# Performance work log

Hardware: AMD Instinct MI355X
Metric: run time of the kernel (lower is better)

Reference implementation:

```python
import jax, jax.numpy as jnp
import numpy as np

BN_EPS = 1e-5


def setup_inputs() -> dict:
    key = jax.random.key(0)
    ks = jax.random.split(key, 8)
    N, E, D, G, L = 50000, 800000, 128, 64, 4
    x = jax.random.normal(ks[0], (N, D), dtype=jnp.float32)
    edge_index = jax.random.randint(ks[1], (2, E), 0, N, dtype=jnp.int64)
    batch = jnp.sort(jax.random.randint(ks[2], (N,), 0, G, dtype=jnp.int64))
    sc = 1.0 / np.sqrt(D)
    W1 = jax.random.normal(ks[3], (L, D, D), dtype=jnp.float32) * sc
    b1 = jnp.zeros((L, D), dtype=jnp.float32)
    gamma = jnp.ones((L, D), dtype=jnp.float32)
    beta = jnp.zeros((L, D), dtype=jnp.float32)
    W2 = jax.random.normal(ks[4], (L, D, D), dtype=jnp.float32) * sc
    b2 = jnp.zeros((L, D), dtype=jnp.float32)
    return {"x": x, "edge_index": edge_index, "batch": batch,
            "W1": W1, "b1": b1, "gamma": gamma, "beta": beta,
            "W2": W2, "b2": b2}


def _segment_mean(vals, ids, num_segments):
    s = jax.ops.segment_sum(vals, ids, num_segments=num_segments)
    cnt = jax.ops.segment_sum(jnp.ones((vals.shape[0],), vals.dtype), ids,
                              num_segments=num_segments)
    return s / jnp.clip(cnt, 1.0)[:, None]


def reference(x, edge_index, batch, W1, b1, gamma, beta, W2, b2):
    N = x.shape[0]
    L = W1.shape[0]
    G = 64  # number of graphs
    src, dst = edge_index[0], edge_index[1]  # source_to_target flow
    # in-degree counts for scatter-mean (fixed across layers)
    deg = jax.ops.segment_sum(jnp.ones((src.shape[0],), x.dtype), dst,
                              num_segments=N)
    deg = jnp.clip(deg, 1.0)[:, None]
    h = x
    node_pool = jnp.zeros((N, W1.shape[2]), x.dtype)
    g_pool = jnp.zeros((G, W1.shape[2]), x.dtype)
    for l in range(L):
        # scatter-mean neighbor aggregation, GIN update with eps=0
        agg = jax.ops.segment_sum(h[src], dst, num_segments=N) / deg
        z = h + agg
        # MLP: Linear -> BatchNorm1d (batch stats) -> ReLU -> Linear
        z = z @ W1[l] + b1[l]
        mu = jnp.mean(z, axis=0)
        var = jnp.mean(jnp.square(z - mu), axis=0)  # biased, as in torch BN
        z = gamma[l] * (z - mu) * jax.lax.rsqrt(var + BN_EPS) + beta[l]
        z = jax.nn.relu(z)
        h = z @ W2[l] + b2[l]
        node_pool = node_pool + h
        g_pool = g_pool + _segment_mean(h, batch, G)
    return node_pool, g_pool
```

## Files before the change

kernel.cpp:

```cpp
#include <hip/hip_runtime.h>

#define D 128
#define GNUM 64
#define LNUM 4
#define BN_EPS 1e-5f
#define EPB 16384
#define SH_MAX 12544

typedef short bf16x8 __attribute__((ext_vector_type(8)));
typedef float f32x4 __attribute__((ext_vector_type(4)));
typedef unsigned short u16x8 __attribute__((ext_vector_type(8)));
typedef unsigned short u16x4 __attribute__((ext_vector_type(4)));

__device__ __forceinline__ float bf2f(unsigned short u) {
  union { unsigned int i; float f; } v; v.i = ((unsigned int)u) << 16; return v.f;
}
__device__ __forceinline__ unsigned short f2bf(float f) {
  union { float f; unsigned int i; } v; v.f = f;
  unsigned int b = v.i;
  return (unsigned short)((b + 0x7FFFu + ((b >> 16) & 1u)) >> 16);
}

__global__ __launch_bounds__(256) void k_hist(const int* __restrict__ ei, int E,
                                              int B, int nbin, int* __restrict__ hist) {
  __shared__ int lh[256];
  int b = blockIdx.x, tx = threadIdx.x;
  lh[tx] = 0;
  __syncthreads();
  int s = b * EPB, e = min(s + EPB, E);
  for (int j = s + tx; j < e; j += 256) atomicAdd(&lh[ei[(size_t)E + j] >> 8], 1);
  __syncthreads();
  if (tx < nbin) hist[tx * B + b] = lh[tx];
}

__global__ __launch_bounds__(1024) void k_hscan(const int* __restrict__ hist, int M,
                                                int* __restrict__ off,
                                                int* __restrict__ rowptr, int N, int E) {
  __shared__ int sh[SH_MAX];
  __shared__ int sh2[1024];
  int tx = threadIdx.x;
  int chunk = (M + 1023) / 1024;
  for (int i = 0; i < chunk; ++i) {
    int idx = tx * chunk + i;
    sh[idx] = (idx < M) ? hist[idx] : 0;
  }
  __syncthreads();
  int s = 0;
  for (int i = 0; i < chunk; ++i) s += sh[tx * chunk + i];
  sh2[tx] = s;
  __syncthreads();
  for (int o = 1; o < 1024; o <<= 1) {
    int u = (tx >= o) ? sh2[tx - o] : 0;
    __syncthreads();
    sh2[tx] += u;
    __syncthreads();
  }
  int run = (tx == 0) ? 0 : sh2[tx - 1];
  for (int i = 0; i < chunk; ++i) {
    int idx = tx * chunk + i;
    if (idx < M) { int v = sh[idx]; off[idx] = run; run += v; }
  }
  if (tx == 0) rowptr[N] = E;
}

__global__ __launch_bounds__(256) void k_scatter(const int* __restrict__ ei, int E,
                                                 int B, int nbin,
                                                 const int* __restrict__ off,
                                                 int2* __restrict__ sorted) {
  __shared__ int cur[256];
  int b = blockIdx.x, tx = threadIdx.x;
  if (tx < nbin) cur[tx] = off[tx * B + b];
  __syncthreads();
  int s = b * EPB, e = min(s + EPB, E);
  for (int j = s + tx; j < e; j += 256) {
    int d = ei[(size_t)E + j];
    int sc = ei[j];
    int p = atomicAdd(&cur[d >> 8], 1);
    sorted[p] = make_int2(d, sc);
  }
}

__global__ __launch_bounds__(256) void k_build(const int2* __restrict__ sorted,
                                               const int* __restrict__ off,
                                               int B, int nbin, int E, int N,
                                               int* __restrict__ rowptr,
                                               int* __restrict__ col) {
  __shared__ int cnt[256], excl[256], cur[256];
  int beta = blockIdx.x, tx = threadIdx.x;
  int s = off[beta * B];
  int e = (beta + 1 < nbin) ? off[(beta + 1) * B] : E;
  cnt[tx] = 0;
  __syncthreads();
  for (int j = s + tx; j < e; j += 256) atomicAdd(&cnt[sorted[j].x & 255], 1);
  __syncthreads();
  int v = cnt[tx];
  excl[tx] = v;
  __syncthreads();
  for (int o = 1; o < 256; o <<= 1) {
    int u = (tx >= o) ? excl[tx - o] : 0;
    __syncthreads();
    excl[tx] += u;
    __syncthreads();
  }
  int ex = excl[tx] - v;
  int n = beta * 256 + tx;
  if (n < N) rowptr[n] = s + ex;
  cur[tx] = s + ex;
  __syncthreads();
  for (int j = s + tx; j < e; j += 256) {
    int2 p = sorted[j];
    int q = atomicAdd(&cur[p.x & 255], 1);
    col[q] = p.y;
  }
}

__global__ void k_bounds(const int* __restrict__ batch, int N, int* __restrict__ bound) {
  int g = threadIdx.x;
  if (g > GNUM) return;
  int lo = 0, hi = N;
  while (lo < hi) { int mid = (lo + hi) >> 1; if (batch[mid] < g) lo = mid + 1; else hi = mid; }
  bound[g] = lo;
}

__global__ void k_prep_x(const float* __restrict__ x, unsigned short* __restrict__ hx, int total4) {
  int i = blockIdx.x * 256 + threadIdx.x;
  if (i < total4) {
    f32x4 v = ((const f32x4*)x)[i];
    u16x4 o; o[0] = f2bf(v[0]); o[1] = f2bf(v[1]); o[2] = f2bf(v[2]); o[3] = f2bf(v[3]);
    ((u16x4*)hx)[i] = o;
  }
}

__global__ __launch_bounds__(256) void k_prep_w(const float* __restrict__ W1,
                                                const float* __restrict__ W2,
                                                unsigned short* __restrict__ wt) {
  int l = blockIdx.x;
  const float* W = (l < LNUM) ? (W1 + (size_t)l * D * D) : (W2 + (size_t)(l - LNUM) * D * D);
  unsigned short* o = wt + (size_t)l * D * D;
#pragma unroll
  for (int i = 0; i < 64; ++i) {
    int idx = threadIdx.x + 256 * i;
    int k = idx >> 7, n = idx & 127;
    o[n * D + k] = f2bf(W[idx]);
  }
}

__global__ __launch_bounds__(256) void k_layer1(const unsigned short* __restrict__ hin,
                                                const int* __restrict__ rowptr,
                                                const int* __restrict__ col,
                                                const unsigned short* __restrict__ wt,
                                                const float* __restrict__ bias,
                                                unsigned short* __restrict__ t,
                                                float* __restrict__ partials, int N) {
  __shared__ union { unsigned short zt[64 * D]; float red[2 * 8 * D]; } uA;
  __shared__ union { unsigned short wl[D * D]; float out[64 * D]; } uB;
  int tx = threadIdx.x;
  int r0 = blockIdx.x * 64;
  const u16x8* wg = (const u16x8*)wt;
#pragma unroll
  for (int i = 0; i < 8; ++i) {
    int cid = tx + 256 * i;
    int row = cid >> 4, c16 = cid & 15;
    u16x8 v = wg[cid];
    *(u16x8*)((char*)uB.wl + row * 256 + ((c16 * 16) ^ ((row & 7) << 4))) = v;
  }
  int grp = tx >> 4, c = tx & 15;
  const u16x8* h8 = (const u16x8*)hin;
#pragma unroll
  for (int i = 0; i < 4; ++i) {
    int row = grp * 4 + i;
    int n = r0 + row;
    u16x8 o;
    if (n < N) {
      int e0 = rowptr[n], e1 = rowptr[n + 1];
      f32x4 s0 = {0.f,0.f,0.f,0.f}, s1 = {0.f,0.f,0.f,0.f};
      f32x4 t0 = {0.f,0.f,0.f,0.f}, t1 = {0.f,0.f,0.f,0.f};
      int j = e0;
      for (; j + 3 < e1; j += 4) {
        u16x8 v0 = h8[(size_t)col[j] * 16 + c];
        u16x8 v1 = h8[(size_t)col[j + 1] * 16 + c];
        u16x8 v2 = h8[(size_t)col[j + 2] * 16 + c];
        u16x8 v3 = h8[(size_t)col[j + 3] * 16 + c];
#pragma unroll
        for (int k = 0; k < 4; ++k) {
          s0[k] += bf2f(v0[k]) + bf2f(v1[k]);
          s1[k] += bf2f(v0[4 + k]) + bf2f(v1[4 + k]);
          t0[k] += bf2f(v2[k]) + bf2f(v3[k]);
          t1[k] += bf2f(v2[4 + k]) + bf2f(v3[4 + k]);
        }
      }
      for (; j < e1; ++j) {
        u16x8 v0 = h8[(size_t)col[j] * 16 + c];
#pragma unroll
        for (int k = 0; k < 4; ++k) { s0[k] += bf2f(v0[k]); s1[k] += bf2f(v0[4 + k]); }
      }
      s0 += t0; s1 += t1;
      float inv = (e1 > e0) ? 1.f / (float)(e1 - e0) : 0.f;
      u16x8 hv = h8[(size_t)n * 16 + c];
#pragma unroll
      for (int k = 0; k < 4; ++k) {
        o[k] = f2bf(bf2f(hv[k]) + s0[k] * inv);
        o[4 + k] = f2bf(bf2f(hv[4 + k]) + s1[k] * inv);
      }
    } else {
      o = (u16x8){0, 0, 0, 0, 0, 0, 0, 0};
    }
    *(u16x8*)((char*)uA.zt + row * 256 + ((c * 16) ^ ((row & 7) << 4))) = o;
  }
  __syncthreads();
  int l = tx & 63, w = tx >> 6;
  int lm = l & 15, lg = l >> 4;
  f32x4 acc[8];
#pragma unroll
  for (int cc = 0; cc < 8; ++cc) { float bv = bias[cc * 16 + lm]; acc[cc] = (f32x4){bv, bv, bv, bv}; }
  int arow = 16 * w + lm;
  const char* zb = (const char*)uA.zt + arow * 256;
  int aswz = (arow & 7) << 4;
#pragma unroll
  for (int kt = 0; kt < 4; ++kt) {
    int koff = kt * 64 + lg * 16;
    bf16x8 af = *(const bf16x8*)(zb + (koff ^ aswz));
#pragma unroll
    for (int cc = 0; cc < 8; ++cc) {
      int n = cc * 16 + lm;
      bf16x8 bfr = *(const bf16x8*)((const char*)uB.wl + n * 256 + (koff ^ ((n & 7) << 4)));
      acc[cc] = __builtin_amdgcn_mfma_f32_16x16x32_bf16(af, bfr, acc[cc], 0, 0, 0);
    }
  }
  __syncthreads();
#pragma unroll
  for (int cc = 0; cc < 8; ++cc)
#pragma unroll
    for (int r = 0; r < 4; ++r)
      uB.out[(16 * w + 4 * lg + r) * D + cc * 16 + lm] = acc[cc][r];
  __syncthreads();
  int tc = tx & 31, tr = tx >> 5;
  f32x4 s = {0.f, 0.f, 0.f, 0.f}, q = {0.f, 0.f, 0.f, 0.f};
#pragma unroll
  for (int i = 0; i < 8; ++i) {
    int row = i * 8 + tr;
    f32x4 v = *(f32x4*)&uB.out[row * D + tc * 4];
    u16x4 o; o[0] = f2bf(v[0]); o[1] = f2bf(v[1]); o[2] = f2bf(v[2]); o[3] = f2bf(v[3]);
    *(u16x4*)(t + (size_t)(r0 + row) * D + tc * 4) = o;
    if (r0 + row < N) { s += v; q += v * v; }
  }
  *(f32x4*)&uA.red[tr * D + tc * 4] = s;
  *(f32x4*)&uA.red[8 * D + tr * D + tc * 4] = q;
  __syncthreads();
  int colx = tx & 127, which = tx >> 7;
  float S = 0.f;
#pragma unroll
  for (int j = 0; j < 8; ++j) S += uA.red[which * 8 * D + j * D + colx];
  partials[(size_t)blockIdx.x * 256 + tx] = S;
}

__global__ __launch_bounds__(256) void k_red1(const float* __restrict__ partials, int NB,
                                              float* __restrict__ partial2) {
  int tx = threadIdx.x;
  float S = 0.f;
  for (int b = blockIdx.x; b < NB; b += 64) S += partials[(size_t)b * 256 + tx];
  partial2[(size_t)blockIdx.x * 256 + tx] = S;
}

__global__ __launch_bounds__(256) void k_finalize(const float* __restrict__ partial2,
                                                  const float* __restrict__ gamma,
                                                  const float* __restrict__ beta,
                                                  float* __restrict__ stats, int N) {
  __shared__ float sh[256];
  int tx = threadIdx.x;
  float S = 0.f;
#pragma unroll 8
  for (int b = 0; b < 64; ++b) S += partial2[(size_t)b * 256 + tx];
  sh[tx] = S;
  __syncthreads();
  if (tx < D) {
    float mu = sh[tx] / (float)N;
    float var = sh[D + tx] / (float)N - mu * mu;
    float rstd = rsqrtf(fmaxf(var, 0.f) + BN_EPS);
    float A = gamma[tx] * rstd;
    stats[tx] = A;
    stats[D + tx] = beta[tx] - mu * A;
  }
}

__device__ __forceinline__ void gemm2_core(const unsigned short* t,
                                           const unsigned short* wt,
                                           const float* bias, const float* stats,
                                           unsigned short* at, unsigned short* wl,
                                           float* outbuf, int r0) {
  int tx = threadIdx.x;
  const u16x8* tg = (const u16x8*)(t + (size_t)r0 * D);
#pragma unroll
  for (int i = 0; i < 4; ++i) {
    int cid = tx + 256 * i;
    int row = cid >> 4, c16 = cid & 15;
    u16x8 v = tg[cid];
    int c0 = c16 * 8;
    f32x4 a0 = *(const f32x4*)&stats[c0];
    f32x4 a1 = *(const f32x4*)&stats[c0 + 4];
    f32x4 b0 = *(const f32x4*)&stats[D + c0];
    f32x4 b1v = *(const f32x4*)&stats[D + c0 + 4];
    u16x8 o;
    o[0] = f2bf(fmaxf(bf2f(v[0]) * a0[0] + b0[0], 0.f));
    o[1] = f2bf(fmaxf(bf2f(v[1]) * a0[1] + b0[1], 0.f));
    o[2] = f2bf(fmaxf(bf2f(v[2]) * a0[2] + b0[2], 0.f));
    o[3] = f2bf(fmaxf(bf2f(v[3]) * a0[3] + b0[3], 0.f));
    o[4] = f2bf(fmaxf(bf2f(v[4]) * a1[0] + b1v[0], 0.f));
    o[5] = f2bf(fmaxf(bf2f(v[5]) * a1[1] + b1v[1], 0.f));
    o[6] = f2bf(fmaxf(bf2f(v[6]) * a1[2] + b1v[2], 0.f));
    o[7] = f2bf(fmaxf(bf2f(v[7]) * a1[3] + b1v[3], 0.f));
    *(u16x8*)((char*)at + row * 256 + ((c16 * 16) ^ ((row & 7) << 4))) = o;
  }
  const u16x8* wg = (const u16x8*)wt;
#pragma unroll
  for (int i = 0; i < 8; ++i) {
    int cid = tx + 256 * i;
    int row = cid >> 4, c16 = cid & 15;
    u16x8 v = wg[cid];
    *(u16x8*)((char*)wl + row * 256 + ((c16 * 16) ^ ((row & 7) << 4))) = v;
  }
  __syncthreads();
  int l = tx & 63, w = tx >> 6;
  int lm = l & 15, lg = l >> 4;
  f32x4 acc[8];
#pragma unroll
  for (int c = 0; c < 8; ++c) { float bv = bias[c * 16 + lm]; acc[c] = (f32x4){bv, bv, bv, bv}; }
  int arow = 16 * w + lm;
  const char* ab = (const char*)at + arow * 256;
  int aswz = (arow & 7) << 4;
#pragma unroll
  for (int kt = 0; kt < 4; ++kt) {
    int koff = kt * 64 + lg * 16;
    bf16x8 af = *(const bf16x8*)(ab + (koff ^ aswz));
#pragma unroll
    for (int c = 0; c < 8; ++c) {
      int n = c * 16 + lm;
      bf16x8 bfr = *(const bf16x8*)((const char*)wl + n * 256 + (koff ^ ((n & 7) << 4)));
      acc[c] = __builtin_amdgcn_mfma_f32_16x16x32_bf16(af, bfr, acc[c], 0, 0, 0);
    }
  }
  __syncthreads();
#pragma unroll
  for (int c = 0; c < 8; ++c)
#pragma unroll
    for (int r = 0; r < 4; ++r)
      outbuf[(16 * w + 4 * lg + r) * D + c * 16 + lm] = acc[c][r];
  __syncthreads();
}

__global__ __launch_bounds__(256) void k_gemm2(const unsigned short* __restrict__ t,
                                               const unsigned short* __restrict__ wt,
                                               const float* __restrict__ bias,
                                               const float* __restrict__ stats,
                                               unsigned short* __restrict__ h, int N) {
  __shared__ unsigned short at[64 * D];
  __shared__ union { unsigned short wl[D * D]; float out[64 * D]; } uB;
  int tx = threadIdx.x;
  int r0 = blockIdx.x * 64;
  gemm2_core(t, wt, bias, stats, at, uB.wl, uB.out, r0);
  int tc = tx & 31, tr = tx >> 5;
#pragma unroll
  for (int i = 0; i < 8; ++i) {
    int row = i * 8 + tr;
    int gr = r0 + row;
    if (gr < N) {
      f32x4 v = *(f32x4*)&uB.out[row * D + tc * 4];
      u16x4 hb; hb[0] = f2bf(v[0]); hb[1] = f2bf(v[1]); hb[2] = f2bf(v[2]); hb[3] = f2bf(v[3]);
      *(u16x4*)(h + (size_t)gr * D + tc * 4) = hb;
    }
  }
}

__global__ __launch_bounds__(256) void k_gemm2_last(const unsigned short* __restrict__ t,
                                                    const unsigned short* __restrict__ wt,
                                                    const float* __restrict__ bias,
                                                    const float* __restrict__ stats,
                                                    const unsigned short* __restrict__ h0,
                                                    const unsigned short* __restrict__ h1,
                                                    const unsigned short* __restrict__ h2,
                                                    float* __restrict__ np, int N) {
  __shared__ unsigned short at[64 * D];
  __shared__ union { unsigned short wl[D * D]; float out[64 * D]; } uB;
  int tx = threadIdx.x;
  int r0 = blockIdx.x * 64;
  gemm2_core(t, wt, bias, stats, at, uB.wl, uB.out, r0);
  int tc = tx & 31, tr = tx >> 5;
#pragma unroll
  for (int i = 0; i < 8; ++i) {
    int row = i * 8 + tr;
    int gr = r0 + row;
    if (gr < N) {
      f32x4 v = *(f32x4*)&uB.out[row * D + tc * 4];
      size_t o4 = (size_t)gr * D + tc * 4;
      u16x4 a = *(const u16x4*)(h0 + o4);
      u16x4 b = *(const u16x4*)(h1 + o4);
      u16x4 cc = *(const u16x4*)(h2 + o4);
      f32x4 o;
#pragma unroll
      for (int k = 0; k < 4; ++k)
        o[k] = v[k] + (bf2f(a[k]) + bf2f(b[k])) + bf2f(cc[k]);
      *(f32x4*)(np + o4) = o;
    }
  }
}

__global__ __launch_bounds__(256) void k_gpool(const float* __restrict__ np,
                                               const int* __restrict__ bound,
                                               float* __restrict__ gp) {
  __shared__ float red[8 * D];
  int g = blockIdx.x;
  int s = bound[g], e = bound[g + 1];
  int tc = threadIdx.x & 31, tr = threadIdx.x >> 5;
  f32x4 a = {0.f, 0.f, 0.f, 0.f};
  for (int r = s + tr; r < e; r += 8)
    a += *(const f32x4*)(np + (size_t)r * D + tc * 4);
  *(f32x4*)&red[tr * D + tc * 4] = a;
  __syncthreads();
  if (threadIdx.x < D) {
    float v = 0.f;
#pragma unroll
    for (int j = 0; j < 8; ++j) v += red[j * D + threadIdx.x];
    float c = (float)(e - s);
    gp[(size_t)g * D + threadIdx.x] = v / fmaxf(c, 1.f);
  }
}

extern "C" void kernel_launch(void* const* d_in, const int* in_sizes, int n_in,
                              void* d_out, int out_size, void* d_ws,
                              size_t ws_size, hipStream_t stream) {
  const float* x = (const float*)d_in[0];
  const int* ei = (const int*)d_in[1];
  const int* batch = (const int*)d_in[2];
  const float* W1 = (const float*)d_in[3];
  const float* b1 = (const float*)d_in[4];
  const float* gamma = (const float*)d_in[5];
  const float* beta = (const float*)d_in[6];
  const float* W2 = (const float*)d_in[7];
  const float* b2 = (const float*)d_in[8];
  int N = in_sizes[0] / D;
  int E = in_sizes[1] / 2;
  int Npad = (N + 63) & ~63;
  int gb = Npad / 64;
  int B = (E + EPB - 1) / EPB;
  int nbin = (N + 255) / 256;
  int M = nbin * B;

  float* out = (float*)d_out;
  float* node_pool = out;
  float* g_pool = out + (size_t)N * D;

  char* wp = (char*)d_ws;
  unsigned short* hx = (unsigned short*)wp;   wp += (size_t)Npad * D * 2;
  unsigned short* t = (unsigned short*)wp;    wp += (size_t)Npad * D * 2;
  unsigned short* hbuf[3];
  for (int l = 0; l < 3; ++l) { hbuf[l] = (unsigned short*)wp; wp += (size_t)Npad * D * 2; }
  unsigned short* wt = (unsigned short*)wp;   wp += (size_t)8 * D * D * 2;
  float* partials = (float*)wp;               wp += (size_t)gb * 256 * 4;
  float* partial2 = (float*)wp;               wp += (size_t)64 * 256 * 4;
  float* stats = (float*)wp;                  wp += (size_t)2 * D * 4;
  int* bound = (int*)wp;                      wp += (size_t)(GNUM + 4) * 4;
  int* rowptr = (int*)wp;                     wp += (size_t)(N + 1) * 4;
  int* hist = (int*)wp;                       wp += (size_t)SH_MAX * 4;
  int* off = (int*)wp;                        wp += (size_t)SH_MAX * 4;
  int* col = (int*)wp;                        wp += (size_t)E * 4;
  int2* sorted = (int2*)wp;                   wp += (size_t)E * 8;

  k_prep_w<<<8, 256, 0, stream>>>(W1, W2, wt);
  k_prep_x<<<(N * 32 + 255) / 256, 256, 0, stream>>>(x, hx, N * 32);
  k_hist<<<B, 256, 0, stream>>>(ei, E, B, nbin, hist);
  k_hscan<<<1, 1024, 0, stream>>>(hist, M, off, rowptr, N, E);
  k_scatter<<<B, 256, 0, stream>>>(ei, E, B, nbin, off, sorted);
  k_build<<<nbin, 256, 0, stream>>>(sorted, off, B, nbin, E, N, rowptr, col);
  k_bounds<<<1, 128, 0, stream>>>(batch, N, bound);

  for (int ll = 0; ll < LNUM; ++ll) {
    const unsigned short* hin = (ll == 0) ? hx : hbuf[ll - 1];
    k_layer1<<<gb, 256, 0, stream>>>(hin, rowptr, col, wt + (size_t)ll * D * D,
                                     b1 + (size_t)ll * D, t, partials, N);
    k_red1<<<64, 256, 0, stream>>>(partials, gb, partial2);
    k_finalize<<<1, 256, 0, stream>>>(partial2, gamma + (size_t)ll * D,
                                      beta + (size_t)ll * D, stats, N);
    if (ll < LNUM - 1) {
      k_gemm2<<<gb, 256, 0, stream>>>(t, wt + (size_t)(LNUM + ll) * D * D,
                                      b2 + (size_t)ll * D, stats, hbuf[ll], N);
    } else {
      k_gemm2_last<<<gb, 256, 0, stream>>>(t, wt + (size_t)(LNUM + ll) * D * D,
                                           b2 + (size_t)ll * D, stats,
                                           hbuf[0], hbuf[1], hbuf[2], node_pool, N);
    }
  }
  k_gpool<<<GNUM, 256, 0, stream>>>(node_pool, bound, g_pool);
}
```

Before: 458.7 us.

## Gather neighbor aggregates directly into MFMA A-fragments, skipping LDS staging

The layer-1 kernel now has each MFMA lane gather and average the neighbor features for exactly the row and k-slices it feeds into the MFMA, keeping the results in registers as A-fragments. This removes the shared-memory z tile, its write/read round trip and one barrier, and shrinks LDS use. In exchange, each lane now walks a whole node's edge list on its own, reading four 16-byte chunks per edge with less coalescing across lanes. Per-lane register pressure also rises.

```diff
diff --git a/kernel.cpp b/kernel.cpp
--- a/kernel.cpp
+++ b/kernel.cpp
@@ -152,8 +152,8 @@
                                                 const float* __restrict__ bias,
                                                 unsigned short* __restrict__ t,
                                                 float* __restrict__ partials, int N) {
-  __shared__ union { unsigned short zt[64 * D]; float red[2 * 8 * D]; } uA;
   __shared__ union { unsigned short wl[D * D]; float out[64 * D]; } uB;
+  __shared__ float red[2 * 8 * D];
   int tx = threadIdx.x;
   int r0 = blockIdx.x * 64;
   const u16x8* wg = (const u16x8*)wt;
@@ -164,67 +164,77 @@
     u16x8 v = wg[cid];
     *(u16x8*)((char*)uB.wl + row * 256 + ((c16 * 16) ^ ((row & 7) << 4))) = v;
   }
-  int grp = tx >> 4, c = tx & 15;
-  const u16x8* h8 = (const u16x8*)hin;
-#pragma unroll
-  for (int i = 0; i < 4; ++i) {
-    int row = grp * 4 + i;
-    int n = r0 + row;
-    u16x8 o;
-    if (n < N) {
-      int e0 = rowptr[n], e1 = rowptr[n + 1];
-      f32x4 s0 = {0.f,0.f,0.f,0.f}, s1 = {0.f,0.f,0.f,0.f};
-      f32x4 t0 = {0.f,0.f,0.f,0.f}, t1 = {0.f,0.f,0.f,0.f};
-      int j = e0;
-      for (; j + 3 < e1; j += 4) {
-        u16x8 v0 = h8[(size_t)col[j] * 16 + c];
-        u16x8 v1 = h8[(size_t)col[j + 1] * 16 + c];
-        u16x8 v2 = h8[(size_t)col[j + 2] * 16 + c];
-        u16x8 v3 = h8[(size_t)col[j + 3] * 16 + c];
-#pragma unroll
-        for (int k = 0; k < 4; ++k) {
-          s0[k] += bf2f(v0[k]) + bf2f(v1[k]);
-          s1[k] += bf2f(v0[4 + k]) + bf2f(v1[4 + k]);
-          t0[k] += bf2f(v2[k]) + bf2f(v3[k]);
-          t1[k] += bf2f(v2[4 + k]) + bf2f(v3[4 + k]);
-        }
-      }
-      for (; j < e1; ++j) {
-        u16x8 v0 = h8[(size_t)col[j] * 16 + c];
-#pragma unroll
-        for (int k = 0; k < 4; ++k) { s0[k] += bf2f(v0[k]); s1[k] += bf2f(v0[4 + k]); }
-      }
-      s0 += t0; s1 += t1;
-      float inv = (e1 > e0) ? 1.f / (float)(e1 - e0) : 0.f;
-      u16x8 hv = h8[(size_t)n * 16 + c];
-#pragma unroll
-      for (int k = 0; k < 4; ++k) {
-        o[k] = f2bf(bf2f(hv[k]) + s0[k] * inv);
-        o[4 + k] = f2bf(bf2f(hv[4 + k]) + s1[k] * inv);
-      }
-    } else {
-      o = (u16x8){0, 0, 0, 0, 0, 0, 0, 0};
-    }
-    *(u16x8*)((char*)uA.zt + row * 256 + ((c * 16) ^ ((row & 7) << 4))) = o;
-  }
-  __syncthreads();
   int l = tx & 63, w = tx >> 6;
   int lm = l & 15, lg = l >> 4;
+  int row = 16 * w + lm;
+  int n = r0 + row;
+  const u16x8* h8 = (const u16x8*)hin;
+  f32x4 sA[4] = {{0.f,0.f,0.f,0.f},{0.f,0.f,0.f,0.f},{0.f,0.f,0.f,0.f},{0.f,0.f,0.f,0.f}};
+  f32x4 sB[4] = {{0.f,0.f,0.f,0.f},{0.f,0.f,0.f,0.f},{0.f,0.f,0.f,0.f},{0.f,0.f,0.f,0.f}};
+  int e0 = 0, e1 = 0;
+  if (n < N) { e0 = rowptr[n]; e1 = rowptr[n + 1]; }
+  int j = e0;
+  for (; j + 1 < e1; j += 2) {
+    size_t c0 = (size_t)col[j] * 16 + lg;
+    size_t c1 = (size_t)col[j + 1] * 16 + lg;
+    u16x8 v00 = h8[c0];      u16x8 v01 = h8[c0 + 4];
+    u16x8 v02 = h8[c0 + 8];  u16x8 v03 = h8[c0 + 12];
+    u16x8 v10 = h8[c1];      u16x8 v11 = h8[c1 + 4];
+    u16x8 v12 = h8[c1 + 8];  u16x8 v13 = h8[c1 + 12];
+#pragma unroll
+    for (int k = 0; k < 4; ++k) {
+      sA[0][k] += bf2f(v00[k]) + bf2f(v10[k]);
+      sB[0][k] += bf2f(v00[4 + k]) + bf2f(v10[4 + k]);
+      sA[1][k] += bf2f(v01[k]) + bf2f(v11[k]);
+      sB[1][k] += bf2f(v01[4 + k]) + bf2f(v11[4 + k]);
+      sA[2][k] += bf2f(v02[k]) + bf2f(v12[k]);
+      sB[2][k] += bf2f(v02[4 + k]) + bf2f(v12[4 + k]);
+      sA[3][k] += bf2f(v03[k]) + bf2f(v13[k]);
+      sB[3][k] += bf2f(v03[4 + k]) + bf2f(v13[4 + k]);
+    }
+  }
+  if (j < e1) {
+    size_t c0 = (size_t)col[j] * 16 + lg;
+    u16x8 v00 = h8[c0];      u16x8 v01 = h8[c0 + 4];
+    u16x8 v02 = h8[c0 + 8];  u16x8 v03 = h8[c0 + 12];
+#pragma unroll
+    for (int k = 0; k < 4; ++k) {
+      sA[0][k] += bf2f(v00[k]);  sB[0][k] += bf2f(v00[4 + k]);
+      sA[1][k] += bf2f(v01[k]);  sB[1][k] += bf2f(v01[4 + k]);
+      sA[2][k] += bf2f(v02[k]);  sB[2][k] += bf2f(v02[4 + k]);
+      sA[3][k] += bf2f(v03[k]);  sB[3][k] += bf2f(v03[4 + k]);
+    }
+  }
+  bf16x8 af[4];
+  if (n < N) {
+    float inv = (e1 > e0) ? 1.f / (float)(e1 - e0) : 0.f;
+#pragma unroll
+    for (int kt = 0; kt < 4; ++kt) {
+      u16x8 hv = h8[(size_t)n * 16 + kt * 4 + lg];
+      u16x8 o;
+#pragma unroll
+      for (int k = 0; k < 4; ++k) {
+        o[k] = f2bf(bf2f(hv[k]) + sA[kt][k] * inv);
+        o[4 + k] = f2bf(bf2f(hv[4 + k]) + sB[kt][k] * inv);
+      }
+      af[kt] = *(bf16x8*)&o;
+    }
+  } else {
+#pragma unroll
+    for (int kt = 0; kt < 4; ++kt) af[kt] = (bf16x8){0,0,0,0,0,0,0,0};
+  }
+  __syncthreads();
   f32x4 acc[8];
 #pragma unroll
   for (int cc = 0; cc < 8; ++cc) { float bv = bias[cc * 16 + lm]; acc[cc] = (f32x4){bv, bv, bv, bv}; }
-  int arow = 16 * w + lm;
-  const char* zb = (const char*)uA.zt + arow * 256;
-  int aswz = (arow & 7) << 4;
 #pragma unroll
   for (int kt = 0; kt < 4; ++kt) {
     int koff = kt * 64 + lg * 16;
-    bf16x8 af = *(const bf16x8*)(zb + (koff ^ aswz));
 #pragma unroll
     for (int cc = 0; cc < 8; ++cc) {
-      int n = cc * 16 + lm;
-      bf16x8 bfr = *(const bf16x8*)((const char*)uB.wl + n * 256 + (koff ^ ((n & 7) << 4)));
-      acc[cc] = __builtin_amdgcn_mfma_f32_16x16x32_bf16(af, bfr, acc[cc], 0, 0, 0);
+      int nn = cc * 16 + lm;
+      bf16x8 bfr = *(const bf16x8*)((const char*)uB.wl + nn * 256 + (koff ^ ((nn & 7) << 4)));
+      acc[cc] = __builtin_amdgcn_mfma_f32_16x16x32_bf16(af[kt], bfr, acc[cc], 0, 0, 0);
     }
   }
   __syncthreads();
@@ -238,19 +248,19 @@
   f32x4 s = {0.f, 0.f, 0.f, 0.f}, q = {0.f, 0.f, 0.f, 0.f};
 #pragma unroll
   for (int i = 0; i < 8; ++i) {
-    int row = i * 8 + tr;
-    f32x4 v = *(f32x4*)&uB.out[row * D + tc * 4];
+    int rr = i * 8 + tr;
+    f32x4 v = *(f32x4*)&uB.out[rr * D + tc * 4];
     u16x4 o; o[0] = f2bf(v[0]); o[1] = f2bf(v[1]); o[2] = f2bf(v[2]); o[3] = f2bf(v[3]);
-    *(u16x4*)(t + (size_t)(r0 + row) * D + tc * 4) = o;
-    if (r0 + row < N) { s += v; q += v * v; }
-  }
-  *(f32x4*)&uA.red[tr * D + tc * 4] = s;
-  *(f32x4*)&uA.red[8 * D + tr * D + tc * 4] = q;
+    *(u16x4*)(t + (size_t)(r0 + rr) * D + tc * 4) = o;
+    if (r0 + rr < N) { s += v; q += v * v; }
+  }
+  *(f32x4*)&red[tr * D + tc * 4] = s;
+  *(f32x4*)&red[8 * D + tr * D + tc * 4] = q;
   __syncthreads();
   int colx = tx & 127, which = tx >> 7;
   float S = 0.f;
 #pragma unroll
-  for (int j = 0; j < 8; ++j) S += uA.red[which * 8 * D + j * D + colx];
+  for (int jj = 0; jj < 8; ++jj) S += red[which * 8 * D + jj * D + colx];
   partials[(size_t)blockIdx.x * 256 + tx] = S;
 }
 
```

Result: faster. 428.0 us (-6.7%).
